# Optimization experiments

Hardware: AMD Instinct MI355X
Metric: run time of the kernel (lower is better)

Reference implementation:

```python
import jax, jax.numpy as jnp
import numpy as np

HEADS = 8
DIM_HEAD = 64
INNER = HEADS * DIM_HEAD  # 512
QUERY_DIM = 512
CONTEXT_DIM = 512


def setup_inputs() -> dict:
    key = jax.random.key(0)
    ks = jax.random.split(key, 10)
    s_in = 1.0 / np.sqrt(QUERY_DIM)
    s_ctx = 1.0 / np.sqrt(CONTEXT_DIM)
    s_o = 1.0 / np.sqrt(INNER)
    return {
        "x": jax.random.normal(ks[0], (8, QUERY_DIM, 32, 32), jnp.float32),
        "context": jax.random.normal(ks[1], (8, CONTEXT_DIM, 32, 32), jnp.float32),
        "Wq": jax.random.normal(ks[2], (INNER, QUERY_DIM), jnp.float32) * s_in,
        "bq": jnp.zeros((INNER,), jnp.float32),
        "Wk": jax.random.normal(ks[3], (INNER, CONTEXT_DIM), jnp.float32) * s_ctx,
        "bk": jnp.zeros((INNER,), jnp.float32),
        "Wv": jax.random.normal(ks[4], (INNER, CONTEXT_DIM), jnp.float32) * s_ctx,
        "bv": jnp.zeros((INNER,), jnp.float32),
        "Wo": jax.random.normal(ks[5], (QUERY_DIM, INNER), jnp.float32) * s_o,
        "bo": jnp.zeros((QUERY_DIM,), jnp.float32),
    }


def _proj1x1(t, W, b):
    # 1x1 Conv2d: channel mixing only. t: [B,Cin,X,Y], W: [Cout,Cin]
    return jnp.einsum('bcxy,oc->boxy', t, W) + b[None, :, None, None]


def reference(x, context, Wq, bq, Wk, bk, Wv, bv, Wo, bo):
    b, c, h, w = x.shape
    scale = DIM_HEAD ** (-0.5)

    q = _proj1x1(x, Wq, bq)
    k = _proj1x1(context, Wk, bk)
    v = _proj1x1(context, Wv, bv)

    def split_heads(t):
        B, C, X, Y = t.shape  # C = HEADS*DIM_HEAD
        return t.reshape(B, HEADS, DIM_HEAD, X * Y)  # b h d n

    q = split_heads(q) * scale
    k = split_heads(k)
    v = split_heads(v)

    sim = jnp.einsum('bhdi,bhdj->bhij', q, k)          # [b,h,i,j]
    attn = jax.nn.softmax(sim, axis=-1)
    out = jnp.einsum('bhij,bhdj->bhid', attn, v)       # [b,h,i,d]
    # rearrange 'b h (x y) d -> b (h d) x y'
    out = out.transpose(0, 1, 3, 2).reshape(b, HEADS * DIM_HEAD, h, w)
    return _proj1x1(out, Wo, bo)
```

## Files before the change

kernel.cpp:

```cpp
#include <hip/hip_runtime.h>
#include <stdint.h>

#define NB   8
#define CH   512
#define NPIX 1024
#define DH   64

typedef float  f32x4  __attribute__((ext_vector_type(4)));
typedef float  f32x16 __attribute__((ext_vector_type(16)));
typedef __bf16 bf16x8 __attribute__((ext_vector_type(8)));
typedef unsigned int u32x4 __attribute__((ext_vector_type(4)));

static __device__ __forceinline__ unsigned short f2bf(float f) {
    unsigned int u = __builtin_bit_cast(unsigned int, f);
    u += 0x7FFFu + ((u >> 16) & 1u);
    return (unsigned short)(u >> 16);
}

static __device__ __forceinline__ bf16x8 ld_bf8(const unsigned short* p) {
    return *reinterpret_cast<const bf16x8*>(p);
}

static __device__ __forceinline__ unsigned int cvtpk_bf16(float lo, float hi) {
    unsigned int r;
    asm("v_cvt_pk_bf16_f32 %0,%1,%2" : "=v"(r) : "v"(lo), "v"(hi));
    return r;
}

static __device__ __forceinline__ float fexp2(float x) {
    float r;
    asm("v_exp_f32 %0, %1" : "=v"(r) : "v"(x));
    return r;
}

static __device__ __forceinline__ void plswap(unsigned int& a, unsigned int& b) {
    asm("v_permlane32_swap_b32 %0, %1" : "+v"(a), "+v"(b));
}

static __device__ __forceinline__ void glds16(const unsigned short* g, void* l) {
    __builtin_amdgcn_global_load_lds(
        (const __attribute__((address_space(1))) unsigned int*)g,
        (__attribute__((address_space(3))) unsigned int*)l,
        16, 0, 0);
}

#define WAIT_VMCNT_8() asm volatile("s_waitcnt vmcnt(8)" ::: "memory")
#define WAIT_VMCNT_4() asm volatile("s_waitcnt vmcnt(4)" ::: "memory")
#define WAIT_VMCNT_0() asm volatile("s_waitcnt vmcnt(0)" ::: "memory")
#define WAIT_LGKM_0()  asm volatile("s_waitcnt lgkmcnt(0)" ::: "memory")

__global__ __launch_bounds__(256) void wconv_kernel(
        const float* __restrict__ Wq, const float* __restrict__ Wk,
        const float* __restrict__ Wv, const float* __restrict__ Wo,
        unsigned short* __restrict__ out) {
    int idx = blockIdx.x * 256 + threadIdx.x;
    int which = idx >> 18;
    int off   = idx & 0x3FFFF;
    const float* src = which == 0 ? Wq : which == 1 ? Wk : which == 2 ? Wv : Wo;
    out[idx] = f2bf(src[off]);
}

__global__ __launch_bounds__(256) void tconv_kernel(
        const float* __restrict__ x, const float* __restrict__ ctx,
        unsigned short* __restrict__ XT, unsigned short* __restrict__ CT) {
    __shared__ float tile[32][33];
    const int z = blockIdx.z;
    const float* src = (z < 8) ? x : ctx;
    unsigned short* dst = (z < 8) ? XT : CT;
    const int b  = z & 7;
    const int c0 = blockIdx.x * 32, n0 = blockIdx.y * 32;
    const int t  = threadIdx.x;
    const int r  = t >> 3, ch4 = (t & 7) * 4;
    const float* s = src + (size_t)b * CH * NPIX + (size_t)(c0 + r) * NPIX + n0 + ch4;
    float4 v4 = *(const float4*)s;
    tile[r][ch4] = v4.x; tile[r][ch4 + 1] = v4.y;
    tile[r][ch4 + 2] = v4.z; tile[r][ch4 + 3] = v4.w;
    __syncthreads();
    unsigned int lo = ((unsigned)f2bf(tile[ch4 + 1][r]) << 16) | f2bf(tile[ch4][r]);
    unsigned int hw = ((unsigned)f2bf(tile[ch4 + 3][r]) << 16) | f2bf(tile[ch4 + 2][r]);
    *(uint2*)(dst + (size_t)b * NPIX * CH + (size_t)(n0 + r) * CH + c0 + ch4)
        = make_uint2(lo, hw);
}

static __device__ __forceinline__ void gemm128(
        const unsigned short* __restrict__ Wp,
        const unsigned short* __restrict__ Xp,
        f32x4 acc[4][4]) {
    __shared__ __align__(16) unsigned short lA[3][128][32];
    __shared__ __align__(16) unsigned short lB[3][128][32];
    const int tid  = threadIdx.x;
    const int lane = tid & 63;
    const int wv   = tid >> 6;
    const int wm   = wv & 1, wn = tid >> 7;

    const unsigned short* gA = Wp + (size_t)(wv * 32 + (lane >> 2)) * CH + (lane & 3) * 8;
    const unsigned short* gB = Xp + (size_t)(wv * 32 + (lane >> 2)) * CH + (lane & 3) * 8;

    auto stage = [&](int kt, int buf) {
        const int k0 = kt * 32;
        char* dA = (char*)&lA[buf][0][0] + wv * 2048;
        char* dB = (char*)&lB[buf][0][0] + wv * 2048;
        glds16(gA + k0,           dA);
        glds16(gA + k0 + 16 * CH, dA + 1024);
        glds16(gB + k0,           dB);
        glds16(gB + k0 + 16 * CH, dB + 1024);
    };

    stage(0, 0);
    stage(1, 1);

#pragma unroll 1
    for (int kt = 0; kt < 16; kt++) {
        if (kt < 15) { WAIT_VMCNT_4(); } else { WAIT_VMCNT_0(); }
        __builtin_amdgcn_s_barrier();
        if (kt + 2 < 16) stage(kt + 2, (kt + 2) % 3);
        const int buf = kt % 3;
        bf16x8 af[4], bfrag[4];
#pragma unroll
        for (int i = 0; i < 4; i++)
            af[i] = ld_bf8(&lA[buf][wm * 64 + i * 16 + (lane & 15)][(lane >> 4) * 8]);
#pragma unroll
        for (int j = 0; j < 4; j++)
            bfrag[j] = ld_bf8(&lB[buf][wn * 64 + j * 16 + (lane & 15)][(lane >> 4) * 8]);
#pragma unroll
        for (int i = 0; i < 4; i++)
#pragma unroll
            for (int j = 0; j < 4; j++)
                acc[i][j] = __builtin_amdgcn_mfma_f32_16x16x32_bf16(af[i], bfrag[j], acc[i][j], 0, 0, 0);
    }
}

__global__ __launch_bounds__(256) void proj_qkv_kernel(
        const unsigned short* __restrict__ XT, const unsigned short* __restrict__ CT,
        const unsigned short* __restrict__ Wbf,
        const float* __restrict__ bq, const float* __restrict__ bk, const float* __restrict__ bv,
        unsigned short* __restrict__ Q, unsigned short* __restrict__ K, unsigned short* __restrict__ V) {
    const int id = blockIdx.x;
    const int b = id & 7, mode = id >> 8, inner = (id >> 3) & 31;
    const int o0 = (inner & 3) * 128, n0 = (inner >> 2) * 128;
    const unsigned short* W = Wbf + (size_t)mode * CH * CH;
    const unsigned short* X = (mode == 0 ? XT : CT) + (size_t)b * NPIX * CH;
    const float* bias = mode == 0 ? bq : mode == 1 ? bk : bv;

    f32x4 acc[4][4];
#pragma unroll
    for (int i = 0; i < 4; i++)
#pragma unroll
        for (int j = 0; j < 4; j++)
#pragma unroll
            for (int r = 0; r < 4; r++) acc[i][j][r] = 0.f;

    gemm128(W + (size_t)o0 * CH, X + (size_t)n0 * CH, acc);

    const int lane = threadIdx.x & 63;
    const int wm = (threadIdx.x >> 6) & 1, wn = threadIdx.x >> 7;
    const float qs = 0.125f * 1.44269504088896340736f;
#pragma unroll
    for (int i = 0; i < 4; i++) {
        const int ob = o0 + wm * 64 + i * 16 + (lane >> 4) * 4;
        const int h = ob >> 6, dd = ob & 63;
        float b4[4];
#pragma unroll
        for (int r = 0; r < 4; r++) b4[r] = bias[ob + r];
#pragma unroll
        for (int j = 0; j < 4; j++) {
            const int n = n0 + wn * 64 + j * 16 + (lane & 15);
            float v[4];
#pragma unroll
            for (int r = 0; r < 4; r++) v[r] = acc[i][j][r] + b4[r];
            if (mode == 0) {
#pragma unroll
                for (int r = 0; r < 4; r++) v[r] *= qs;
            }
            if (mode <= 1) {
                unsigned int lo = (unsigned)f2bf(v[0]) | ((unsigned)f2bf(v[1]) << 16);
                unsigned int hi = (unsigned)f2bf(v[2]) | ((unsigned)f2bf(v[3]) << 16);
                unsigned short* dst = (mode == 0 ? Q : K) +
                    (((size_t)(b * 8 + h) * NPIX) + n) * DH + dd;
                *(uint2*)dst = make_uint2(lo, hi);
            } else {
#pragma unroll
                for (int r = 0; r < 4; r++) {
                    int d = dd + r;
                    V[(((size_t)(b * 8 + h) * 32 + (n >> 5)) * 2048)
                      + (size_t)(d & 31) * 64 + (d >> 5) * 32 + (n & 31)] = f2bf(v[r]);
                }
            }
        }
    }
}

__global__ __launch_bounds__(128) void attn_kernel(
        const unsigned short* __restrict__ Qg, const unsigned short* __restrict__ Kg,
        const unsigned short* __restrict__ Vg, unsigned short* __restrict__ AT) {
    __shared__ __align__(16) unsigned short ldsS[2][2][2][2048];
    __shared__ float lbuf[64];

    const int p  = blockIdx.x;
    const int local = p >> 3;
    const int bh = ((p & 7) << 3) | (local >> 4);
    const int qb = local & 15;
    const int q0 = qb * 64;
    const int tid = threadIdx.x, wave = tid >> 6, lane = tid & 63;
    const int lq = lane & 31, hi = lane >> 5, lql7 = lq & 7;
    const int key0 = wave * 512;

    const unsigned short* Qp = Qg + ((size_t)bh * NPIX + q0 + lq) * DH + hi * 8;
    bf16x8 qa[4], qbf[4];
#pragma unroll
    for (int ds = 0; ds < 4; ds++) {
        qa[ds]  = ld_bf8(Qp + ds * 16);
        qbf[ds] = ld_bf8(Qp + 32 * DH + ds * 16);
    }

    f32x16 oA0, oA1, oB0, oB1, zro;
#pragma unroll
    for (int r = 0; r < 16; r++) {
        oA0[r] = 0.f; oA1[r] = 0.f; oB0[r] = 0.f; oB1[r] = 0.f; zro[r] = 0.f;
    }
    float lA = 0.f, lB = 0.f;

    const int swz = (((lane & 7) ^ ((lane >> 3) & 7)) << 3);
    const unsigned short* gK = Kg + ((size_t)bh * NPIX + key0 + (lane >> 3)) * DH + swz;
    const unsigned short* gV = Vg + (size_t)bh * 65536 + (size_t)(key0 >> 5) * 2048
                                  + (lane >> 3) * 64 + swz;

    auto stage = [&](int t, int buf) {
        const unsigned short* sk = gK + (size_t)t * 32 * DH;
        char* dK = (char*)&ldsS[wave][buf][0][0];
        glds16(sk,           dK);
        glds16(sk +  8 * DH, dK + 1024);
        glds16(sk + 16 * DH, dK + 2048);
        glds16(sk + 24 * DH, dK + 3072);
        const unsigned short* sv = gV + (size_t)t * 2048;
        char* dV = (char*)&ldsS[wave][buf][1][0];
        glds16(sv,        dV);
        glds16(sv +  512, dV + 1024);
        glds16(sv + 1024, dV + 2048);
        glds16(sv + 1536, dV + 3072);
    };

    stage(0, 0);
    stage(1, 1);

#pragma unroll 1
    for (int t = 0; t < 16; ++t) {
        if (t < 15) { WAIT_VMCNT_8(); } else { WAIT_VMCNT_0(); }
        const int cur = t & 1;
        const unsigned short* kb = &ldsS[wave][cur][0][0] + lq * 64;
        bf16x8 kf0 = ld_bf8(kb + (((0 + hi) ^ lql7) << 3));
        bf16x8 kf1 = ld_bf8(kb + (((2 + hi) ^ lql7) << 3));
        bf16x8 kf2 = ld_bf8(kb + (((4 + hi) ^ lql7) << 3));
        bf16x8 kf3 = ld_bf8(kb + (((6 + hi) ^ lql7) << 3));
        const unsigned short* vb = &ldsS[wave][cur][1][0] + lq * 64;
        bf16x8 v00 = ld_bf8(vb + (((0 + hi) ^ lql7) << 3));
        bf16x8 v01 = ld_bf8(vb + (((2 + hi) ^ lql7) << 3));
        bf16x8 v10 = ld_bf8(vb + (((4 + hi) ^ lql7) << 3));
        bf16x8 v11 = ld_bf8(vb + (((6 + hi) ^ lql7) << 3));

        f32x16 sA, sB;
        __builtin_amdgcn_s_setprio(1);
        sA = __builtin_amdgcn_mfma_f32_32x32x16_bf16(kf0, qa[0],  zro, 0, 0, 0);
        sB = __builtin_amdgcn_mfma_f32_32x32x16_bf16(kf0, qbf[0], zro, 0, 0, 0);
        sA = __builtin_amdgcn_mfma_f32_32x32x16_bf16(kf1, qa[1],  sA, 0, 0, 0);
        sB = __builtin_amdgcn_mfma_f32_32x32x16_bf16(kf1, qbf[1], sB, 0, 0, 0);
        sA = __builtin_amdgcn_mfma_f32_32x32x16_bf16(kf2, qa[2],  sA, 0, 0, 0);
        sB = __builtin_amdgcn_mfma_f32_32x32x16_bf16(kf2, qbf[2], sB, 0, 0, 0);
        sA = __builtin_amdgcn_mfma_f32_32x32x16_bf16(kf3, qa[3],  sA, 0, 0, 0);
        sB = __builtin_amdgcn_mfma_f32_32x32x16_bf16(kf3, qbf[3], sB, 0, 0, 0);
        __builtin_amdgcn_s_setprio(0);

        WAIT_LGKM_0();
        __builtin_amdgcn_sched_barrier(0);
        if (t + 2 < 16) stage(t + 2, cur);
        __builtin_amdgcn_sched_barrier(0);

#pragma unroll
        for (int r = 0; r < 16; r++) { sA[r] = fexp2(sA[r]); sB[r] = fexp2(sB[r]); }
        {
            float a8[8], b8[8], a4[4], b4[4];
#pragma unroll
            for (int i = 0; i < 8; i++) { a8[i] = sA[2*i] + sA[2*i+1]; b8[i] = sB[2*i] + sB[2*i+1]; }
#pragma unroll
            for (int i = 0; i < 4; i++) { a4[i] = a8[2*i] + a8[2*i+1]; b4[i] = b8[2*i] + b8[2*i+1]; }
            lA += (a4[0] + a4[1]) + (a4[2] + a4[3]);
            lB += (b4[0] + b4[1]) + (b4[2] + b4[3]);
        }

        bf16x8 paA[2], paB[2];
#pragma unroll
        for (int ks = 0; ks < 2; ks++) {
            const int bse = ks * 8;
            unsigned int X0 = cvtpk_bf16(sA[bse + 0], sA[bse + 1]);
            unsigned int X1 = cvtpk_bf16(sA[bse + 2], sA[bse + 3]);
            unsigned int X2 = cvtpk_bf16(sA[bse + 4], sA[bse + 5]);
            unsigned int X3 = cvtpk_bf16(sA[bse + 6], sA[bse + 7]);
            plswap(X0, X2); plswap(X1, X3);
            u32x4 wa; wa[0] = X0; wa[1] = X1; wa[2] = X2; wa[3] = X3;
            paA[ks] = __builtin_bit_cast(bf16x8, wa);
            unsigned int Y0 = cvtpk_bf16(sB[bse + 0], sB[bse + 1]);
            unsigned int Y1 = cvtpk_bf16(sB[bse + 2], sB[bse + 3]);
            unsigned int Y2 = cvtpk_bf16(sB[bse + 4], sB[bse + 5]);
            unsigned int Y3 = cvtpk_bf16(sB[bse + 6], sB[bse + 7]);
            plswap(Y0, Y2); plswap(Y1, Y3);
            u32x4 wb; wb[0] = Y0; wb[1] = Y1; wb[2] = Y2; wb[3] = Y3;
            paB[ks] = __builtin_bit_cast(bf16x8, wb);
        }

        __builtin_amdgcn_s_setprio(1);
        oA0 = __builtin_amdgcn_mfma_f32_32x32x16_bf16(paA[0], v00, oA0, 0, 0, 0);
        oB0 = __builtin_amdgcn_mfma_f32_32x32x16_bf16(paB[0], v00, oB0, 0, 0, 0);
        oA1 = __builtin_amdgcn_mfma_f32_32x32x16_bf16(paA[0], v10, oA1, 0, 0, 0);
        oB1 = __builtin_amdgcn_mfma_f32_32x32x16_bf16(paB[0], v10, oB1, 0, 0, 0);
        oA0 = __builtin_amdgcn_mfma_f32_32x32x16_bf16(paA[1], v01, oA0, 0, 0, 0);
        oB0 = __builtin_amdgcn_mfma_f32_32x32x16_bf16(paB[1], v01, oB0, 0, 0, 0);
        oA1 = __builtin_amdgcn_mfma_f32_32x32x16_bf16(paA[1], v11, oA1, 0, 0, 0);
        oB1 = __builtin_amdgcn_mfma_f32_32x32x16_bf16(paB[1], v11, oB1, 0, 0, 0);
        __builtin_amdgcn_s_setprio(0);
    }

    lA += __shfl_xor(lA, 32);
    lB += __shfl_xor(lB, 32);
    float* obuf = (float*)&ldsS[1][0][0][0];
    if (wave == 1) {
#pragma unroll
        for (int r = 0; r < 16; r++) {
            obuf[(0 * 16 + r) * 64 + lane] = oA0[r];
            obuf[(1 * 16 + r) * 64 + lane] = oA1[r];
            obuf[(2 * 16 + r) * 64 + lane] = oB0[r];
            obuf[(3 * 16 + r) * 64 + lane] = oB1[r];
        }
        if (lane < 32) { lbuf[lq] = lA; lbuf[32 + lq] = lB; }
    }
    __syncthreads();
    if (wave == 0) {
        float invA = 1.0f / (lA + lbuf[lq]);
        float invB = 1.0f / (lB + lbuf[32 + lq]);
        const int b = bh >> 3, h = bh & 7;
#pragma unroll
        for (int r = 0; r < 16; r++) {
            float a0 = oA0[r] + obuf[(0 * 16 + r) * 64 + lane];
            float a1 = oA1[r] + obuf[(1 * 16 + r) * 64 + lane];
            float b0 = oB0[r] + obuf[(2 * 16 + r) * 64 + lane];
            float b1 = oB1[r] + obuf[(3 * 16 + r) * 64 + lane];
            int crow = (r & 3) + 8 * (r >> 2) + 4 * hi;
            float facA = __shfl(invA, crow);
            float facB = __shfl(invB, crow);
            unsigned short* dA = AT + ((size_t)b * NPIX + q0 + crow) * CH + h * 64 + lq;
            dA[0]  = f2bf(a0 * facA);
            dA[32] = f2bf(a1 * facA);
            unsigned short* dB = AT + ((size_t)b * NPIX + q0 + 32 + crow) * CH + h * 64 + lq;
            dB[0]  = f2bf(b0 * facB);
            dB[32] = f2bf(b1 * facB);
        }
    }
}

__global__ __launch_bounds__(256) void proj_out_kernel(
        const unsigned short* __restrict__ AT, const unsigned short* __restrict__ Wo,
        const float* __restrict__ bo, float* __restrict__ out) {
    const int id = blockIdx.x;
    const int b = id & 7, inner = id >> 3;
    const int o0 = (inner & 3) * 128, n0 = (inner >> 2) * 128;
    f32x4 acc[4][4];
#pragma unroll
    for (int i = 0; i < 4; i++)
#pragma unroll
        for (int j = 0; j < 4; j++)
#pragma unroll
            for (int r = 0; r < 4; r++) acc[i][j][r] = 0.f;

    gemm128(Wo + (size_t)o0 * CH, AT + ((size_t)b * NPIX + n0) * CH, acc);

    const int lane = threadIdx.x & 63;
    const int wm = (threadIdx.x >> 6) & 1, wn = threadIdx.x >> 7;
#pragma unroll
    for (int i = 0; i < 4; i++) {
        const int ob = o0 + wm * 64 + i * 16 + (lane >> 4) * 4;
        float b4[4];
#pragma unroll
        for (int r = 0; r < 4; r++) b4[r] = bo[ob + r];
#pragma unroll
        for (int j = 0; j < 4; j++) {
            const int n = n0 + wn * 64 + j * 16 + (lane & 15);
#pragma unroll
            for (int r = 0; r < 4; r++)
                out[((size_t)b * CH + ob + r) * NPIX + n] = acc[i][j][r] + b4[r];
        }
    }
}

extern "C" void kernel_launch(void* const* d_in, const int* in_sizes, int n_in,
                              void* d_out, int out_size, void* d_ws, size_t ws_size,
                              hipStream_t stream) {
    const float* x   = (const float*)d_in[0];
    const float* ctx = (const float*)d_in[1];
    const float* Wq  = (const float*)d_in[2];
    const float* bq  = (const float*)d_in[3];
    const float* Wk  = (const float*)d_in[4];
    const float* bk  = (const float*)d_in[5];
    const float* Wv  = (const float*)d_in[6];
    const float* bv  = (const float*)d_in[7];
    const float* Wo  = (const float*)d_in[8];
    const float* bo  = (const float*)d_in[9];
    float* out = (float*)d_out;

    char* ws = (char*)d_ws;
    unsigned short* XT  = (unsigned short*)(ws);
    unsigned short* CT  = (unsigned short*)(ws + 8388608);
    unsigned short* Wbf = (unsigned short*)(ws + 16777216);
    unsigned short* Q   = (unsigned short*)(ws + 18874368);
    unsigned short* K   = (unsigned short*)(ws + 27262976);
    unsigned short* V   = (unsigned short*)(ws + 35651584);
    unsigned short* AT  = XT;

    wconv_kernel<<<4096, 256, 0, stream>>>(Wq, Wk, Wv, Wo, Wbf);
    tconv_kernel<<<dim3(16, 32, 16), 256, 0, stream>>>(x, ctx, XT, CT);
    proj_qkv_kernel<<<768, 256, 0, stream>>>(XT, CT, Wbf, bq, bk, bv, Q, K, V);
    attn_kernel<<<1024, 128, 0, stream>>>(Q, K, V, AT);
    proj_out_kernel<<<256, 256, 0, stream>>>(AT, Wbf + 3 * 262144, bo, out);
}
```

Baseline: 85.78 us.

## Merge weight and input conversion kernels; stagger A/B softmax with PV MFMAs

The weight bf16 conversion and the input transpose-conversion become one launch, with the weight part vectorised to float4 per thread, which removes a kernel launch and its tail. In the attention loop, the two score chains are issued back to back instead of interleaved. The softmax and PV MFMAs for tile A are then issued before the exp and pack work for tile B, so B's VALU exp work can overlap A's MFMAs. Issuing each accumulator chain back to back exposes more MFMA dependency latency in exchange.

After: 82.42 us. 1.04x faster.

```diff
diff --git a/kernel.cpp b/kernel.cpp
--- a/kernel.cpp
+++ b/kernel.cpp
@@ -49,26 +49,32 @@
 #define WAIT_VMCNT_0() asm volatile("s_waitcnt vmcnt(0)" ::: "memory")
 #define WAIT_LGKM_0()  asm volatile("s_waitcnt lgkmcnt(0)" ::: "memory")
 
-__global__ __launch_bounds__(256) void wconv_kernel(
+__global__ __launch_bounds__(256) void prep_kernel(
         const float* __restrict__ Wq, const float* __restrict__ Wk,
         const float* __restrict__ Wv, const float* __restrict__ Wo,
-        unsigned short* __restrict__ out) {
-    int idx = blockIdx.x * 256 + threadIdx.x;
-    int which = idx >> 18;
-    int off   = idx & 0x3FFFF;
-    const float* src = which == 0 ? Wq : which == 1 ? Wk : which == 2 ? Wv : Wo;
-    out[idx] = f2bf(src[off]);
-}
-
-__global__ __launch_bounds__(256) void tconv_kernel(
+        unsigned short* __restrict__ Wbf,
         const float* __restrict__ x, const float* __restrict__ ctx,
         unsigned short* __restrict__ XT, unsigned short* __restrict__ CT) {
     __shared__ float tile[32][33];
-    const int z = blockIdx.z;
+    const int bid = blockIdx.x;
+    if (bid < 1024) {
+        int idx4 = (bid * 256 + threadIdx.x) * 4;
+        int which = idx4 >> 18;
+        int off   = idx4 & 0x3FFFF;
+        const float* src = which == 0 ? Wq : which == 1 ? Wk : which == 2 ? Wv : Wo;
+        float4 v = *(const float4*)(src + off);
+        unsigned int lo = ((unsigned)f2bf(v.y) << 16) | f2bf(v.x);
+        unsigned int hi = ((unsigned)f2bf(v.w) << 16) | f2bf(v.z);
+        *(uint2*)(Wbf + idx4) = make_uint2(lo, hi);
+        return;
+    }
+    const int t0 = bid - 1024;
+    const int z  = t0 >> 9;
+    const int cx = t0 & 15, ny = (t0 >> 4) & 31;
     const float* src = (z < 8) ? x : ctx;
     unsigned short* dst = (z < 8) ? XT : CT;
     const int b  = z & 7;
-    const int c0 = blockIdx.x * 32, n0 = blockIdx.y * 32;
+    const int c0 = cx * 32, n0 = ny * 32;
     const int t  = threadIdx.x;
     const int r  = t >> 3, ch4 = (t & 7) * 4;
     const float* s = src + (size_t)b * CH * NPIX + (size_t)(c0 + r) * NPIX + n0 + ch4;
@@ -261,12 +267,12 @@
         f32x16 sA, sB;
         __builtin_amdgcn_s_setprio(1);
         sA = __builtin_amdgcn_mfma_f32_32x32x16_bf16(kf0, qa[0],  zro, 0, 0, 0);
+        sA = __builtin_amdgcn_mfma_f32_32x32x16_bf16(kf1, qa[1],  sA, 0, 0, 0);
+        sA = __builtin_amdgcn_mfma_f32_32x32x16_bf16(kf2, qa[2],  sA, 0, 0, 0);
+        sA = __builtin_amdgcn_mfma_f32_32x32x16_bf16(kf3, qa[3],  sA, 0, 0, 0);
         sB = __builtin_amdgcn_mfma_f32_32x32x16_bf16(kf0, qbf[0], zro, 0, 0, 0);
-        sA = __builtin_amdgcn_mfma_f32_32x32x16_bf16(kf1, qa[1],  sA, 0, 0, 0);
         sB = __builtin_amdgcn_mfma_f32_32x32x16_bf16(kf1, qbf[1], sB, 0, 0, 0);
-        sA = __builtin_amdgcn_mfma_f32_32x32x16_bf16(kf2, qa[2],  sA, 0, 0, 0);
         sB = __builtin_amdgcn_mfma_f32_32x32x16_bf16(kf2, qbf[2], sB, 0, 0, 0);
-        sA = __builtin_amdgcn_mfma_f32_32x32x16_bf16(kf3, qa[3],  sA, 0, 0, 0);
         sB = __builtin_amdgcn_mfma_f32_32x32x16_bf16(kf3, qbf[3], sB, 0, 0, 0);
         __builtin_amdgcn_s_setprio(0);
 
@@ -276,18 +282,16 @@
         __builtin_amdgcn_sched_barrier(0);
 
 #pragma unroll
-        for (int r = 0; r < 16; r++) { sA[r] = fexp2(sA[r]); sB[r] = fexp2(sB[r]); }
+        for (int r = 0; r < 16; r++) sA[r] = fexp2(sA[r]);
         {
-            float a8[8], b8[8], a4[4], b4[4];
-#pragma unroll
-            for (int i = 0; i < 8; i++) { a8[i] = sA[2*i] + sA[2*i+1]; b8[i] = sB[2*i] + sB[2*i+1]; }
-#pragma unroll
-            for (int i = 0; i < 4; i++) { a4[i] = a8[2*i] + a8[2*i+1]; b4[i] = b8[2*i] + b8[2*i+1]; }
+            float a8[8], a4[4];
+#pragma unroll
+            for (int i = 0; i < 8; i++) a8[i] = sA[2*i] + sA[2*i+1];
+#pragma unroll
+            for (int i = 0; i < 4; i++) a4[i] = a8[2*i] + a8[2*i+1];
             lA += (a4[0] + a4[1]) + (a4[2] + a4[3]);
-            lB += (b4[0] + b4[1]) + (b4[2] + b4[3]);
-        }
-
-        bf16x8 paA[2], paB[2];
+        }
+        bf16x8 paA[2];
 #pragma unroll
         for (int ks = 0; ks < 2; ks++) {
             const int bse = ks * 8;
@@ -298,6 +302,29 @@
             plswap(X0, X2); plswap(X1, X3);
             u32x4 wa; wa[0] = X0; wa[1] = X1; wa[2] = X2; wa[3] = X3;
             paA[ks] = __builtin_bit_cast(bf16x8, wa);
+        }
+
+        __builtin_amdgcn_s_setprio(1);
+        oA0 = __builtin_amdgcn_mfma_f32_32x32x16_bf16(paA[0], v00, oA0, 0, 0, 0);
+        oA1 = __builtin_amdgcn_mfma_f32_32x32x16_bf16(paA[0], v10, oA1, 0, 0, 0);
+        oA0 = __builtin_amdgcn_mfma_f32_32x32x16_bf16(paA[1], v01, oA0, 0, 0, 0);
+        oA1 = __builtin_amdgcn_mfma_f32_32x32x16_bf16(paA[1], v11, oA1, 0, 0, 0);
+        __builtin_amdgcn_s_setprio(0);
+
+#pragma unroll
+        for (int r = 0; r < 16; r++) sB[r] = fexp2(sB[r]);
+        {
+            float b8[8], b4[4];
+#pragma unroll
+            for (int i = 0; i < 8; i++) b8[i] = sB[2*i] + sB[2*i+1];
+#pragma unroll
+            for (int i = 0; i < 4; i++) b4[i] = b8[2*i] + b8[2*i+1];
+            lB += (b4[0] + b4[1]) + (b4[2] + b4[3]);
+        }
+        bf16x8 paB[2];
+#pragma unroll
+        for (int ks = 0; ks < 2; ks++) {
+            const int bse = ks * 8;
             unsigned int Y0 = cvtpk_bf16(sB[bse + 0], sB[bse + 1]);
             unsigned int Y1 = cvtpk_bf16(sB[bse + 2], sB[bse + 3]);
             unsigned int Y2 = cvtpk_bf16(sB[bse + 4], sB[bse + 5]);
@@ -308,13 +335,9 @@
         }
 
         __builtin_amdgcn_s_setprio(1);
-        oA0 = __builtin_amdgcn_mfma_f32_32x32x16_bf16(paA[0], v00, oA0, 0, 0, 0);
         oB0 = __builtin_amdgcn_mfma_f32_32x32x16_bf16(paB[0], v00, oB0, 0, 0, 0);
-        oA1 = __builtin_amdgcn_mfma_f32_32x32x16_bf16(paA[0], v10, oA1, 0, 0, 0);
         oB1 = __builtin_amdgcn_mfma_f32_32x32x16_bf16(paB[0], v10, oB1, 0, 0, 0);
-        oA0 = __builtin_amdgcn_mfma_f32_32x32x16_bf16(paA[1], v01, oA0, 0, 0, 0);
         oB0 = __builtin_amdgcn_mfma_f32_32x32x16_bf16(paB[1], v01, oB0, 0, 0, 0);
-        oA1 = __builtin_amdgcn_mfma_f32_32x32x16_bf16(paA[1], v11, oA1, 0, 0, 0);
         oB1 = __builtin_amdgcn_mfma_f32_32x32x16_bf16(paB[1], v11, oB1, 0, 0, 0);
         __builtin_amdgcn_s_setprio(0);
     }
@@ -414,8 +437,7 @@
     unsigned short* V   = (unsigned short*)(ws + 35651584);
     unsigned short* AT  = XT;
 
-    wconv_kernel<<<4096, 256, 0, stream>>>(Wq, Wk, Wv, Wo, Wbf);
-    tconv_kernel<<<dim3(16, 32, 16), 256, 0, stream>>>(x, ctx, XT, CT);
+    prep_kernel<<<9216, 256, 0, stream>>>(Wq, Wk, Wv, Wo, Wbf, x, ctx, XT, CT);
     proj_qkv_kernel<<<768, 256, 0, stream>>>(XT, CT, Wbf, bq, bk, bv, Q, K, V);
     attn_kernel<<<1024, 128, 0, stream>>>(Q, K, V, AT);
     proj_out_kernel<<<256, 256, 0, stream>>>(AT, Wbf + 3 * 262144, bo, out);
```
